# Kernel optimization log

Hardware: AMD Instinct MI355X
Metric: run time of the kernel (lower is better)

The kernel has to match this reference:

```python
import jax, jax.numpy as jnp
import numpy as np

RX, RY = 8, 2
ANGLES = [0, 90]
M_DIM = N_DIM = 2048


def _make_kernel(rx=RX, ry=RY, angles=ANGLES):
    # Faithful reproduction of GuidedFilterJAX.__init__ kernel construction.
    # For angles that are multiples of 90 deg, scipy ndimage.rotate(order=2,
    # reshape=False) on a square array is exactly np.rot90.
    kernelL = []
    for A in angles:
        k = np.zeros((rx * 4 + 1, rx * 4 + 1), dtype=np.float32)
        if ry == 0:
            k[:, rx * 2] = 1.0
        else:
            k[:, rx * 2 - ry: rx * 2 + ry + 1] = 1.0
        if A % 360 != 0:
            k = np.rot90(k, (A // 90) % 4)
        k = k[rx:3 * rx + 1, rx:3 * rx + 1]
        r = int((k.sum(1) != 0).sum()) // 2 * 2
        c = int((k.sum(0) != 0).sum()) // 2 * 2
        kernelL.append(k[rx - r // 2: rx + r // 2 + 1,
                         rx - c // 2: rx + c // 2 + 1][None, None])
    C = max(kk.shape[-2] for kk in kernelL)
    R = max(kk.shape[-1] for kk in kernelL)
    out = np.zeros((len(angles), 1, C, R), dtype=np.float32)
    for i, kk in enumerate(kernelL):
        dc = (C - kk.shape[-2]) // 2
        dr = (R - kk.shape[-1]) // 2
        out[i, :, dc:dc + kk.shape[-2], dr:dr + kk.shape[-1]] = kk[0, 0]
    return out


def setup_inputs() -> dict:
    key = jax.random.key(0)
    k1, k2 = jax.random.split(key)
    X = jax.random.normal(k1, (1, 1, M_DIM, N_DIM), dtype=jnp.float32)
    y = jax.random.normal(k2, (1, 1, M_DIM, N_DIM), dtype=jnp.float32)
    kernel = jnp.asarray(_make_kernel())  # (AngleNum, 1, c, r)
    return {"X": X, "y": y, "kernel": kernel}


def _boxfilter(x, k, pc, pr):
    # zero-pad then grouped VALID conv (feature_group_count = channels = 1)
    xp = jnp.pad(x, ((0, 0), (0, 0), (pc, pc), (pr, pr)))
    return jax.lax.conv_general_dilated(xp, k, (1, 1), 'VALID',
                                        feature_group_count=x.shape[1])


def reference(X, y, kernel):
    pr, pc = kernel.shape[-1] // 2, kernel.shape[-2] // 2
    ones = jnp.ones_like(X)
    for i in range(kernel.shape[0]):  # small fixed loop over angles
        k = kernel[i:i + 1]
        Ni = _boxfilter(ones, k, pc, pr)          # normalizer (precomputed in orig)
        mean_y = _boxfilter(y, k, pc, pr) / Ni
        mean_x = _boxfilter(X, k, pc, pr) / Ni
        X = X + (mean_y - mean_x)
    return X
```

## Files before the change

kernel.cpp:

```cpp
#include <hip/hip_runtime.h>

#define W 2048
#define H 2048
#define TX 64
#define TY 64
#define HALO 10
#define DW 84
#define DH 84
#define VW 84
#define VH 68

typedef float f4 __attribute__((ext_vector_type(4)));
typedef float f2 __attribute__((ext_vector_type(2)));

__global__ __launch_bounds__(256) void guided_fused(const float* __restrict__ X,
                                                    const float* __restrict__ y,
                                                    float* __restrict__ out) {
    __shared__ float Ds[DH * DW];
    __shared__ float Vs[VH * VW];

    const int tid = threadIdx.x;
    const int i0 = blockIdx.y * TY;
    const int j0 = blockIdx.x * TX;

    for (int c = tid; c < 84 * 21; c += 256) {
        int li = c / 21, k4 = (c - li * 21) * 4;
        int gi = i0 + li - HALO;
        int gj = j0 + k4 - HALO;
        f4 d = {0.f, 0.f, 0.f, 0.f};
        if ((unsigned)gi < H) {
            const float* yp = &y[gi * W + gj];
            const float* xp = &X[gi * W + gj];
            if (gj >= 0 && gj + 3 < W) {
                f2 ya = *(const f2*)yp, yb = *(const f2*)(yp + 2);
                f2 xa = *(const f2*)xp, xb = *(const f2*)(xp + 2);
                d = (f4){ya.x - xa.x, ya.y - xa.y, yb.x - xb.x, yb.y - xb.y};
            } else {
                #pragma unroll
                for (int e = 0; e < 4; ++e) {
                    int g = gj + e;
                    if ((unsigned)g < W) d[e] = yp[e] - xp[e];
                }
            }
        }
        *(f4*)&Ds[li * DW + k4] = d;
    }
    __syncthreads();

    if (tid < 252) {
        int grp = tid % 21, seg = tid / 21;
        int jj = grp * 4, v0 = seg * 6;
        f4 r[22];
        #pragma unroll
        for (int t = 0; t < 22; ++t) {
            int row = v0 + t; if (row > 83) row = 83;
            r[t] = *(const f4*)&Ds[row * DW + jj];
        }
        f4 s = r[0];
        #pragma unroll
        for (int t = 1; t < 17; ++t) s += r[t];
        #pragma unroll
        for (int k = 0; k < 6; ++k) {
            int v = v0 + k;
            if (v < VH) *(f4*)&Vs[v * VW + jj] = s;
            if (k < 5) s += r[k + 17] - r[k];
        }
    }
    __syncthreads();

    for (int c = tid; c < VH * 20; c += 256) {
        int v = c / 20, g4 = (c - v * 20) * 4;
        int gi = i0 + v - 2;
        if ((unsigned)gi >= H) continue;
        f4 a = *(const f4*)&Vs[v * VW + g4];
        f4 b = *(const f4*)&Vs[v * VW + g4 + 4];
        float m = a.y + a.z + a.w + b.x;
        float s0 = m + a.x;
        float s1 = m + b.y;
        float s2 = a.z + a.w + b.x + b.y + b.z;
        float s3 = a.w + b.x + b.y + b.z + b.w;
        int r0 = gi - 8 > 0 ? gi - 8 : 0, r1 = gi + 8 < H - 1 ? gi + 8 : H - 1;
        float rowsN = (float)(r1 - r0 + 1);
        float corr[4] = {s0, s1, s2, s3};
        #pragma unroll
        for (int k = 0; k < 4; ++k) {
            int gj = j0 + g4 + k - 8;
            if ((unsigned)gj < W) {
                int c0 = gj - 2 > 0 ? gj - 2 : 0, c1 = gj + 2 < W - 1 ? gj + 2 : W - 1;
                corr[k] *= __builtin_amdgcn_rcpf(rowsN * (float)(c1 - c0 + 1));
            } else {
                corr[k] = 0.f;
            }
        }
        int off = (v + 8) * DW + g4 + 2;
        f2 o01 = *(f2*)&Ds[off];
        f2 o23 = *(f2*)&Ds[off + 2];
        o01.x -= corr[0]; o01.y -= corr[1];
        o23.x -= corr[2]; o23.y -= corr[3];
        *(f2*)&Ds[off] = o01;
        *(f2*)&Ds[off + 2] = o23;
    }
    __syncthreads();

    if (tid < 160) {
        int grp = tid % 20, seg = tid / 20;
        int g4 = grp * 4, w0 = seg * 8;
        f4 r[12];
        #pragma unroll
        for (int t = 0; t < 12; ++t) {
            int b = (w0 + 8 + t) * DW + g4 + 2;
            f2 p = *(const f2*)&Ds[b], q = *(const f2*)&Ds[b + 2];
            r[t] = (f4){p.x, p.y, q.x, q.y};
        }
        f4 s = r[0] + r[1] + r[2] + r[3] + r[4];
        #pragma unroll
        for (int k = 0; k < 8; ++k) {
            *(f4*)&Vs[(w0 + k) * VW + g4] = s;
            if (k < 7) s += r[k + 5] - r[k];
        }
    }
    __syncthreads();

    {
        int w = tid >> 2, x0 = (tid & 3) * 16;
        int gi = i0 + w;
        int r0 = gi - 2 > 0 ? gi - 2 : 0, r1 = gi + 2 < H - 1 ? gi + 2 : H - 1;
        float rowsN = (float)(r1 - r0 + 1);
        float val[32];
        #pragma unroll
        for (int q = 0; q < 8; ++q) {
            f4 t = *(const f4*)&Vs[w * VW + x0 + q * 4];
            val[q * 4 + 0] = t.x; val[q * 4 + 1] = t.y;
            val[q * 4 + 2] = t.z; val[q * 4 + 3] = t.w;
        }
        float s = 0.f;
        #pragma unroll
        for (int c = 0; c < 17; ++c) s += val[c];
        #pragma unroll
        for (int xp = 0; xp < 8; ++xp) {
            int x = xp * 2;
            float f01[2];
            #pragma unroll
            for (int e = 0; e < 2; ++e) {
                int gj = j0 + x0 + x + e;
                int c0 = gj - 8 > 0 ? gj - 8 : 0, c1 = gj + 8 < W - 1 ? gj + 8 : W - 1;
                f01[e] = s * __builtin_amdgcn_rcpf(rowsN * (float)(c1 - c0 + 1));
                if (x + e < 15) s += val[x + e + 17] - val[x + e];
            }
            int off = (w + 10) * DW + (x0 + x + 10);
            f2 o = *(f2*)&Ds[off];
            o.x = f01[0] - o.x;
            o.y = f01[1] - o.y;
            *(f2*)&Ds[off] = o;
        }
    }
    __syncthreads();

    #pragma unroll
    for (int k = 0; k < 4; ++k) {
        int idx = tid + k * 256;
        int w = idx >> 4, g = idx & 15;
        int gi = i0 + w, gj = j0 + 4 * g;
        int b = (w + 10) * DW + 4 * g + 10;
        f2 p = *(const f2*)&Ds[b], q = *(const f2*)&Ds[b + 2];
        f4 yv = *(const f4*)&y[gi * W + gj];
        f4 o = {yv.x + p.x, yv.y + p.y, yv.z + q.x, yv.w + q.y};
        *(f4*)&out[gi * W + gj] = o;
    }
}

extern "C" void kernel_launch(void* const* d_in, const int* in_sizes, int n_in,
                              void* d_out, int out_size, void* d_ws, size_t ws_size,
                              hipStream_t stream) {
    const float* X = (const float*)d_in[0];
    const float* y = (const float*)d_in[1];
    float* out = (float*)d_out;

    dim3 blk(256, 1, 1);
    dim3 grd(W / TX, H / TY, 1);
    guided_fused<<<grd, blk, 0, stream>>>(X, y, out);
}
```

Before: 103.3 us.

## Halve tile height and use 512-thread blocks with lighter per-thread work

```diff
diff --git a/kernel.cpp b/kernel.cpp
--- a/kernel.cpp
+++ b/kernel.cpp
@@ -3,19 +3,19 @@
 #define W 2048
 #define H 2048
 #define TX 64
-#define TY 64
+#define TY 32
 #define HALO 10
 #define DW 84
-#define DH 84
+#define DH 52
 #define VW 84
-#define VH 68
+#define VH 36
 
 typedef float f4 __attribute__((ext_vector_type(4)));
 typedef float f2 __attribute__((ext_vector_type(2)));
 
-__global__ __launch_bounds__(256) void guided_fused(const float* __restrict__ X,
-                                                    const float* __restrict__ y,
-                                                    float* __restrict__ out) {
+__global__ __launch_bounds__(512, 6) void guided_fused(const float* __restrict__ X,
+                                                       const float* __restrict__ y,
+                                                       float* __restrict__ out) {
     __shared__ float Ds[DH * DW];
     __shared__ float Vs[VH * VW];
 
@@ -23,7 +23,7 @@
     const int i0 = blockIdx.y * TY;
     const int j0 = blockIdx.x * TX;
 
-    for (int c = tid; c < 84 * 21; c += 256) {
+    for (int c = tid; c < DH * 21; c += 512) {
         int li = c / 21, k4 = (c - li * 21) * 4;
         int gi = i0 + li - HALO;
         int gj = j0 + k4 - HALO;
@@ -47,28 +47,25 @@
     }
     __syncthreads();
 
-    if (tid < 252) {
+    if (tid < 189) {
         int grp = tid % 21, seg = tid / 21;
-        int jj = grp * 4, v0 = seg * 6;
-        f4 r[22];
+        int jj = grp * 4, v0 = seg * 4;
+        const f4* dp = (const f4*)&Ds[v0 * DW + jj];
+        #define DROW(t) dp[(t) * (DW / 4)]
+        f4 r0 = DROW(0), r1 = DROW(1), r2 = DROW(2);
+        f4 s = r0 + r1 + r2;
         #pragma unroll
-        for (int t = 0; t < 22; ++t) {
-            int row = v0 + t; if (row > 83) row = 83;
-            r[t] = *(const f4*)&Ds[row * DW + jj];
-        }
-        f4 s = r[0];
-        #pragma unroll
-        for (int t = 1; t < 17; ++t) s += r[t];
-        #pragma unroll
-        for (int k = 0; k < 6; ++k) {
-            int v = v0 + k;
-            if (v < VH) *(f4*)&Vs[v * VW + jj] = s;
-            if (k < 5) s += r[k + 17] - r[k];
-        }
+        for (int t = 3; t < 17; ++t) s += DROW(t);
+        f4* vp = (f4*)&Vs[v0 * VW + jj];
+        vp[0] = s;
+        s += DROW(17) - r0; vp[VW / 4] = s;
+        s += DROW(18) - r1; vp[2 * (VW / 4)] = s;
+        s += DROW(19) - r2; vp[3 * (VW / 4)] = s;
+        #undef DROW
     }
     __syncthreads();
 
-    for (int c = tid; c < VH * 20; c += 256) {
+    for (int c = tid; c < VH * 20; c += 512) {
         int v = c / 20, g4 = (c - v * 20) * 4;
         int gi = i0 + v - 2;
         if ((unsigned)gi >= H) continue;
@@ -104,31 +101,30 @@
 
     if (tid < 160) {
         int grp = tid % 20, seg = tid / 20;
-        int g4 = grp * 4, w0 = seg * 8;
-        f4 r[12];
-        #pragma unroll
-        for (int t = 0; t < 12; ++t) {
-            int b = (w0 + 8 + t) * DW + g4 + 2;
-            f2 p = *(const f2*)&Ds[b], q = *(const f2*)&Ds[b + 2];
-            r[t] = (f4){p.x, p.y, q.x, q.y};
-        }
-        f4 s = r[0] + r[1] + r[2] + r[3] + r[4];
-        #pragma unroll
-        for (int k = 0; k < 8; ++k) {
-            *(f4*)&Vs[(w0 + k) * VW + g4] = s;
-            if (k < 7) s += r[k + 5] - r[k];
-        }
+        int g4 = grp * 4, w0 = seg * 4;
+        const float* base = &Ds[(w0 + 8) * DW + g4 + 2];
+        #define D2ROW(t) ({ f2 p_ = *(const f2*)&base[(t) * DW]; \
+                            f2 q_ = *(const f2*)&base[(t) * DW + 2]; \
+                            (f4){p_.x, p_.y, q_.x, q_.y}; })
+        f4 r0 = D2ROW(0), r1 = D2ROW(1), r2 = D2ROW(2);
+        f4 s = r0 + r1 + r2 + D2ROW(3) + D2ROW(4);
+        f4* vp = (f4*)&Vs[w0 * VW + g4];
+        vp[0] = s;
+        s += D2ROW(5) - r0; vp[VW / 4] = s;
+        s += D2ROW(6) - r1; vp[2 * (VW / 4)] = s;
+        s += D2ROW(7) - r2; vp[3 * (VW / 4)] = s;
+        #undef D2ROW
     }
     __syncthreads();
 
     {
-        int w = tid >> 2, x0 = (tid & 3) * 16;
+        int w = tid >> 4, x0 = (tid & 15) * 4;
         int gi = i0 + w;
         int r0 = gi - 2 > 0 ? gi - 2 : 0, r1 = gi + 2 < H - 1 ? gi + 2 : H - 1;
         float rowsN = (float)(r1 - r0 + 1);
-        float val[32];
+        float val[20];
         #pragma unroll
-        for (int q = 0; q < 8; ++q) {
+        for (int q = 0; q < 5; ++q) {
             f4 t = *(const f4*)&Vs[w * VW + x0 + q * 4];
             val[q * 4 + 0] = t.x; val[q * 4 + 1] = t.y;
             val[q * 4 + 2] = t.z; val[q * 4 + 3] = t.w;
@@ -136,30 +132,26 @@
         float s = 0.f;
         #pragma unroll
         for (int c = 0; c < 17; ++c) s += val[c];
+        float f[4];
         #pragma unroll
-        for (int xp = 0; xp < 8; ++xp) {
-            int x = xp * 2;
-            float f01[2];
-            #pragma unroll
-            for (int e = 0; e < 2; ++e) {
-                int gj = j0 + x0 + x + e;
-                int c0 = gj - 8 > 0 ? gj - 8 : 0, c1 = gj + 8 < W - 1 ? gj + 8 : W - 1;
-                f01[e] = s * __builtin_amdgcn_rcpf(rowsN * (float)(c1 - c0 + 1));
-                if (x + e < 15) s += val[x + e + 17] - val[x + e];
-            }
-            int off = (w + 10) * DW + (x0 + x + 10);
-            f2 o = *(f2*)&Ds[off];
-            o.x = f01[0] - o.x;
-            o.y = f01[1] - o.y;
-            *(f2*)&Ds[off] = o;
+        for (int x = 0; x < 4; ++x) {
+            int gj = j0 + x0 + x;
+            int c0 = gj - 8 > 0 ? gj - 8 : 0, c1 = gj + 8 < W - 1 ? gj + 8 : W - 1;
+            f[x] = s * __builtin_amdgcn_rcpf(rowsN * (float)(c1 - c0 + 1));
+            if (x < 3) s += val[x + 17] - val[x];
         }
+        int off = (w + 10) * DW + (x0 + 10);
+        f2 o01 = *(f2*)&Ds[off];
+        f2 o23 = *(f2*)&Ds[off + 2];
+        o01.x = f[0] - o01.x; o01.y = f[1] - o01.y;
+        o23.x = f[2] - o23.x; o23.y = f[3] - o23.y;
+        *(f2*)&Ds[off] = o01;
+        *(f2*)&Ds[off + 2] = o23;
     }
     __syncthreads();
 
-    #pragma unroll
-    for (int k = 0; k < 4; ++k) {
-        int idx = tid + k * 256;
-        int w = idx >> 4, g = idx & 15;
+    {
+        int w = tid >> 4, g = tid & 15;
         int gi = i0 + w, gj = j0 + 4 * g;
         int b = (w + 10) * DW + 4 * g + 10;
         f2 p = *(const f2*)&Ds[b], q = *(const f2*)&Ds[b + 2];
@@ -176,7 +168,7 @@
     const float* y = (const float*)d_in[1];
     float* out = (float*)d_out;
 
-    dim3 blk(256, 1, 1);
+    dim3 blk(512, 1, 1);
     dim3 grd(W / TX, H / TY, 1);
     guided_fused<<<grd, blk, 0, stream>>>(X, y, out);
 }
```

Result: faster. 94.68 us (-8.3%).
